# Kernel tuning notes

Measured on AMD Instinct MI355X. Metric: run time of the kernel, lower is better.

## Reference

```python
import jax, jax.numpy as jnp
import numpy as np


def _gcn_layer(h, src, dst, dinv_src_dst, num_nodes, W, b):
    # h: [N, Fin]; src/dst: [E'] (self-loops included); returns [N, Fout]
    h = h @ W  # GCNConv applies the linear transform before propagation
    msg = dinv_src_dst[:, None] * h[src]  # [E', Fout]
    out = jnp.zeros((num_nodes, h.shape[1]), h.dtype).at[dst].add(msg)
    return out + b


def setup_inputs() -> dict:
    key = jax.random.key(0)
    ks = jax.random.split(key, 8)
    N, E, G = 100000, 1600000, 512
    Fin, H, Fout = 1, 64, 16
    x = jax.random.normal(ks[0], (N, Fin), dtype=jnp.float32)
    edge_index = jax.random.randint(ks[1], (2, E), 0, N, dtype=jnp.int64)
    batch = jnp.sort(jax.random.randint(ks[2], (N,), 0, G, dtype=jnp.int64))
    # Glorot-style params (scaled normals are fine for a numerical reference)
    W1 = jax.random.normal(ks[3], (Fin, H), dtype=jnp.float32) / np.sqrt(Fin)
    b1 = jnp.zeros((H,), jnp.float32)
    W2 = jax.random.normal(ks[4], (H, H), dtype=jnp.float32) / np.sqrt(H)
    b2 = jnp.zeros((H,), jnp.float32)
    Wf = jax.random.normal(ks[5], (H, Fout), dtype=jnp.float32) / np.sqrt(H)
    bf = jnp.zeros((Fout,), jnp.float32)
    return {"x": x, "edge_index": edge_index, "batch": batch, "num_graphs": G,
            "W1": W1, "b1": b1, "W2": W2, "b2": b2, "Wf": Wf, "bf": bf}


def reference(x, edge_index, batch, num_graphs, W1, b1, W2, b2, Wf, bf):
    N = x.shape[0]
    loops = jnp.arange(N, dtype=edge_index.dtype)
    src = jnp.concatenate([edge_index[0], loops])  # add self-loops (GCNConv default)
    dst = jnp.concatenate([edge_index[1], loops])
    # symmetric normalization: deg^{-1/2}[src] * deg^{-1/2}[dst]
    deg = jnp.zeros((N,), x.dtype).at[dst].add(1.0)
    dinv = jax.lax.rsqrt(deg)
    norm = dinv[src] * dinv[dst]  # [E']

    h = _gcn_layer(x, src, dst, norm, N, W1, b1)
    h = jax.nn.relu(h)
    h = _gcn_layer(h, src, dst, norm, N, W2, b2)

    # global_mean_pool over batch segments
    sums = jax.ops.segment_sum(h, batch, num_segments=num_graphs)  # [G, H]
    cnts = jax.ops.segment_sum(jnp.ones((N,), h.dtype), batch, num_segments=num_graphs)
    pooled = sums / jnp.maximum(cnts, 1.0)[:, None]
    return pooled @ Wf + bf  # [G, 16]
```

## Files before the change

### kernel.cpp

```cpp
#include <hip/hip_runtime.h>
#include <hip/hip_fp16.h>

#define TPB 256
#define NBUCK 512
#define BCAP 4480
#define A2_BLOCKS 400


__global__ void k_setup(int* cursor, const float* W2, const float* Wf,
                        const float* b2, const float* bf, float* M, float* bb,
                        float* zeroReg, int nzero) {
    int tid = blockIdx.x * blockDim.x + threadIdx.x;
    if (tid < NBUCK) {
        cursor[tid] = tid * BCAP;
    } else if (tid < NBUCK + 1024) {
        int t = tid - NBUCK;
        int f = t >> 4, o = t & 15;
        float a = 0.f;
        for (int k = 0; k < 64; ++k) a = fmaf(W2[f * 64 + k], Wf[k * 16 + o], a);
        M[t] = a;
        if (t < 16) {
            float c = 0.f;
            for (int k = 0; k < 64; ++k) c = fmaf(b2[k], Wf[k * 16 + t], c);
            bb[t] = c + bf[t];
        }
    } else {
        int z = tid - NBUCK - 1024;
        if (z < nzero) zeroReg[z] = 0.f;
    }
}

__global__ void k_bscatter(const int* src, const int* dst, int* bucketCursor,
                           int* packed, int E, int chunk) {
    __shared__ int shc[NBUCK];
    __shared__ int cur[NBUCK];
    int t = threadIdx.x;
    shc[t] = 0; shc[t + 256] = 0;
    __syncthreads();
    int e0 = blockIdx.x * chunk;
    int e1 = min(E, e0 + chunk);
    for (int e = e0 + t; e < e1; e += 256)
        atomicAdd(&shc[dst[e] >> 8], 1);
    __syncthreads();
    int c0 = shc[t], c1 = shc[t + 256];
    if (c0) cur[t] = atomicAdd(&bucketCursor[t], c0);
    if (c1) cur[t + 256] = atomicAdd(&bucketCursor[t + 256], c1);
    __syncthreads();
    for (int e = e0 + t; e < e1; e += 256) {
        int d = dst[e];
        int b = d >> 8;
        int off = atomicAdd(&cur[b], 1);
        if (off < (b + 1) * BCAP)
            packed[off] = ((d & 255) << 24) | src[e];
    }
}

__global__ void k_scan_counts(const int* cursor, int* csrBase) {
    __shared__ int sh[NBUCK];
    int t = threadIdx.x;
    int v = min(cursor[t] - t * BCAP, BCAP);
    sh[t] = v;
    __syncthreads();
    for (int off = 1; off < NBUCK; off <<= 1) {
        int a = (t >= off) ? sh[t - off] : 0;
        __syncthreads();
        sh[t] += a;
        __syncthreads();
    }
    csrBase[t] = sh[t] - v;
    if (t == NBUCK - 1) csrBase[NBUCK] = sh[t];
}

__global__ void k_bucket_csr(const int* cursor, const int* csrBase,
                             const int* packed, const float* x,
                             int* cnt, int* rowStart, float* dinv, float* u,
                             int* csr, int N) {
    __shared__ int c256[256];
    __shared__ int row256[256];
    __shared__ int cur256[256];
    const int b = blockIdx.x;
    const int t = threadIdx.x;
    const int nodeBase = b * 256;
    const int nodeCnt = min(N - nodeBase, 256);
    const int eb = b * BCAP;
    const int ee = min(cursor[b], eb + BCAP);
    const int cb = csrBase[b];

    c256[t] = 0;
    __syncthreads();
    for (int e = eb + t; e < ee; e += 256)
        atomicAdd(&c256[((unsigned)packed[e]) >> 24], 1);
    __syncthreads();

    int v = c256[t];
    row256[t] = v;
    __syncthreads();
    for (int off = 1; off < 256; off <<= 1) {
        int a = (t >= off) ? row256[t - off] : 0;
        __syncthreads();
        row256[t] += a;
        __syncthreads();
    }
    int excl = row256[t] - v;
    cur256[t] = excl;
    __syncthreads();

    if (t < nodeCnt) {
        int i = nodeBase + t;
        cnt[i] = v;
        rowStart[i] = cb + excl;
        float dv = rsqrtf(1.f + (float)v);
        dinv[i] = dv;
        u[i] = dv * x[i];
    }

    for (int e = eb + t; e < ee; e += 256) {
        int w = packed[e];
        int local = ((unsigned)w) >> 24;
        int s = w & 0x00FFFFFF;
        int off = atomicAdd(&cur256[local], 1);
        csr[cb + off] = s;
    }
}

__global__ void k_node(const int* rowStart, const int* cnt, const int* csr,
                       const float* u, const float* dinv,
                       const float* W1, const float* b1, const float* M,
                       __half2* zd, int N) {
    __shared__ float sW1[64], sb1[64], sM[1024];
    int t = threadIdx.x;
    if (t < 64) { sW1[t] = W1[t]; sb1[t] = b1[t]; }
    for (int j = t; j < 1024; j += blockDim.x) sM[j] = M[j];
    __syncthreads();
    int i = blockIdx.x * blockDim.x + t;
    if (i >= N) return;
    float dv = dinv[i];
    int rs = rowStart[i], dg = cnt[i];
    int dgm1 = dg - 1;
    float acc[8];
    acc[0] = u[i];
#pragma unroll
    for (int l = 1; l < 8; ++l) acc[l] = 0.f;
    for (int k = 0; k < dg; k += 16) {
        int sidx[16];
#pragma unroll
        for (int l = 0; l < 16; ++l) sidx[l] = csr[rs + min(k + l, dgm1)];
        float vv[16];
#pragma unroll
        for (int l = 0; l < 16; ++l) vv[l] = u[sidx[l]];
#pragma unroll
        for (int l = 0; l < 16; ++l) acc[l & 7] += (k + l < dg) ? vv[l] : 0.f;
    }
    float s = dv * (((acc[0] + acc[1]) + (acc[2] + acc[3])) +
                    ((acc[4] + acc[5]) + (acc[6] + acc[7])));
    float za[16];
#pragma unroll
    for (int o = 0; o < 16; ++o) za[o] = 0.f;
    for (int f = 0; f < 64; ++f) {
        float hf = fmaxf(fmaf(s, sW1[f], sb1[f]), 0.f);
#pragma unroll
        for (int o = 0; o < 16; ++o) za[o] = fmaf(hf, sM[f * 16 + o], za[o]);
    }
#pragma unroll
    for (int o = 0; o < 8; ++o)
        zd[i * 8 + o] = __floats2half2_rn(dv * za[2 * o], dv * za[2 * o + 1]);
}

__global__ void k_gather_pool(const int* batch, const int* rowStart, const int* cnt,
                              const int* csr, const __half2* zd, const float* dinv,
                              float* gsum, float* cntf, int N) {
    const int t = threadIdx.x;
    const int lane = t & 63, wave = t >> 6;
    const int j = lane & 7, row = lane >> 3;
    const int iw0 = blockIdx.x * 32 + wave * 8;
    const int i = iw0 + row;
    const bool valid = i < N;
    float vx = 0.f, vy = 0.f;
    int g = 0;
    if (valid) {
        g = batch[i];
        int rs = rowStart[i], dg = cnt[i];
        int dgm1 = dg - 1;
        float2 a[8];
        a[0] = __half22float2(zd[i * 8 + j]);
#pragma unroll
        for (int l = 1; l < 8; ++l) a[l] = make_float2(0.f, 0.f);
        for (int k = 0; k < dg; k += 16) {
            int sidx[16];
#pragma unroll
            for (int l = 0; l < 16; ++l) sidx[l] = csr[rs + min(k + l, dgm1)];
            float2 h[16];
#pragma unroll
            for (int l = 0; l < 16; ++l) h[l] = __half22float2(zd[sidx[l] * 8 + j]);
#pragma unroll
            for (int l = 0; l < 16; ++l) {
                bool m = (k + l) < dg;
                a[l & 7].x += m ? h[l].x : 0.f;
                a[l & 7].y += m ? h[l].y : 0.f;
            }
        }
        float dvv = dinv[i];
        vx = dvv * (((a[0].x + a[1].x) + (a[2].x + a[3].x)) +
                    ((a[4].x + a[5].x) + (a[6].x + a[7].x)));
        vy = dvv * (((a[0].y + a[1].y) + (a[2].y + a[3].y)) +
                    ((a[4].y + a[5].y) + (a[6].y + a[7].y)));
    }

    if (iw0 >= N) return;
    const int nvalid = min(N - iw0, 8);
    const int g0 = batch[iw0];
    const int g1 = batch[min(iw0 + 7, N - 1)];

    if (g0 == g1) {
#pragma unroll
        for (int m = 8; m < 64; m <<= 1) {
            vx += __shfl_xor(vx, m);
            vy += __shfl_xor(vy, m);
        }
        if (lane < 8) {
            atomicAdd(&gsum[g0 * 16 + 2 * j],     vx);
            atomicAdd(&gsum[g0 * 16 + 2 * j + 1], vy);
            if (lane == 0) atomicAdd(&cntf[g0], (float)nvalid);
        }
    } else {
        if (valid) {
            atomicAdd(&gsum[g * 16 + 2 * j],     vx);
            atomicAdd(&gsum[g * 16 + 2 * j + 1], vy);
            if (j == 0) atomicAdd(&cntf[g], 1.0f);
        }
    }
}

__global__ void k_final(const float* gsum, const float* cntf, const float* bb,
                        float* out, int G) {
    int t = blockIdx.x * blockDim.x + threadIdx.x;
    int g = t >> 4, o = t & 15;
    if (g >= G) return;
    out[t] = gsum[t] / fmaxf(cntf[g], 1.0f) + bb[o];
}


static inline int cdiv(int a, int b) { return (a + b - 1) / b; }

extern "C" void kernel_launch(void* const* d_in, const int* in_sizes, int n_in,
                              void* d_out, int out_size, void* d_ws, size_t ws_size,
                              hipStream_t stream) {
    const float* x   = (const float*)d_in[0];
    const int*   ei  = (const int*)d_in[1];
    const int*   bat = (const int*)d_in[2];
    const float* W1  = (const float*)d_in[4];
    const float* b1  = (const float*)d_in[5];
    const float* W2  = (const float*)d_in[6];
    const float* b2  = (const float*)d_in[7];
    const float* Wf  = (const float*)d_in[8];
    const float* bf  = (const float*)d_in[9];
    float* out = (float*)d_out;

    const int N = in_sizes[0];
    const int E = in_sizes[1] / 2;
    const int G = out_size / 16;
    const int NB = cdiv(N, 256);

    const int* src = ei;
    const int* dst = ei + E;

    char* w = (char*)d_ws;
    int*   cursor  = (int*)w;           w += NBUCK * 4;
    int*   csrBase = (int*)w;           w += (NBUCK + 1) * 4 + 12;
    int*   packed  = (int*)w;
    __half2* zd    = (__half2*)packed;
    {
        size_t pk = (size_t)NB * BCAP;
        size_t zo = (size_t)8 * N;
        w += (pk > zo ? pk : zo) * 4;
    }
    int*   csr      = (int*)w;          w += (size_t)E * 4;
    int*   cnt      = (int*)w;          w += (size_t)N * 4;
    int*   rowStart = (int*)w;          w += (size_t)N * 4;
    float* dinv     = (float*)w;        w += (size_t)N * 4;
    float* u        = (float*)w;        w += (size_t)N * 4;
    float* gsum     = (float*)w;        w += (size_t)16 * G * 4;
    float* cntf     = (float*)w;        w += (size_t)G * 4;
    float* M        = (float*)w;        w += 1024 * 4;
    float* bb       = (float*)w;

    const int nzero = 16 * G + G;
    const int chunk = cdiv(E, A2_BLOCKS);

    k_setup<<<cdiv(NBUCK + 1024 + nzero, TPB), TPB, 0, stream>>>(
        cursor, W2, Wf, b2, bf, M, bb, gsum, nzero);

    k_bscatter<<<A2_BLOCKS, 256, 0, stream>>>(src, dst, cursor, packed, E, chunk);
    k_scan_counts<<<1, NBUCK, 0, stream>>>(cursor, csrBase);
    k_bucket_csr<<<NB, 256, 0, stream>>>(cursor, csrBase, packed, x,
                                         cnt, rowStart, dinv, u, csr, N);

    k_node<<<cdiv(N, TPB), TPB, 0, stream>>>(rowStart, cnt, csr, u, dinv, W1, b1, M, zd, N);

    k_gather_pool<<<cdiv(N, 32), 256, 0, stream>>>(bat, rowStart, cnt, csr, zd, dinv, gsum, cntf, N);

    k_final<<<cdiv(G * 16, TPB), TPB, 0, stream>>>(gsum, cntf, bb, out, G);
}
```

Before: 109.8 us.

## Replace CSR build with bucket-local push aggregation in shared memory

Drops the prefix-scan and CSR construction kernels and aggregates directly from the destination-bucketed packed edge list. Layer one stages u in four quarter-chunks in LDS and accumulates per destination with shared atomics. Layer two plus pooling scatters half-precision features into a per-bucket LDS accumulator. This removes the CSR writes and the per-node irregular gathers. In exchange it adds heavy shared-memory atomic traffic, rescans the packed list four times, and uses about 100KB of LDS per block, which may limit occupancy.

```diff
diff --git a/kernel.cpp b/kernel.cpp
--- a/kernel.cpp
+++ b/kernel.cpp
@@ -5,6 +5,7 @@
 #define NBUCK 512
 #define BCAP 4480
 #define A2_BLOCKS 400
+#define QMAX 25088
 
 
 __global__ void k_setup(int* cursor, const float* W2, const float* Wf,
@@ -55,104 +56,63 @@
     }
 }
 
-__global__ void k_scan_counts(const int* cursor, int* csrBase) {
-    __shared__ int sh[NBUCK];
-    int t = threadIdx.x;
-    int v = min(cursor[t] - t * BCAP, BCAP);
-    sh[t] = v;
-    __syncthreads();
-    for (int off = 1; off < NBUCK; off <<= 1) {
-        int a = (t >= off) ? sh[t - off] : 0;
-        __syncthreads();
-        sh[t] += a;
-        __syncthreads();
-    }
-    csrBase[t] = sh[t] - v;
-    if (t == NBUCK - 1) csrBase[NBUCK] = sh[t];
-}
-
-__global__ void k_bucket_csr(const int* cursor, const int* csrBase,
-                             const int* packed, const float* x,
-                             int* cnt, int* rowStart, float* dinv, float* u,
-                             int* csr, int N) {
+__global__ void k_bucket1(const int* cursor, const int* packed, const float* x,
+                          float* dinv, float* u, int N) {
     __shared__ int c256[256];
-    __shared__ int row256[256];
-    __shared__ int cur256[256];
-    const int b = blockIdx.x;
-    const int t = threadIdx.x;
-    const int nodeBase = b * 256;
-    const int nodeCnt = min(N - nodeBase, 256);
+    const int b = blockIdx.x, t = threadIdx.x;
     const int eb = b * BCAP;
     const int ee = min(cursor[b], eb + BCAP);
-    const int cb = csrBase[b];
-
     c256[t] = 0;
     __syncthreads();
     for (int e = eb + t; e < ee; e += 256)
         atomicAdd(&c256[((unsigned)packed[e]) >> 24], 1);
     __syncthreads();
-
-    int v = c256[t];
-    row256[t] = v;
-    __syncthreads();
-    for (int off = 1; off < 256; off <<= 1) {
-        int a = (t >= off) ? row256[t - off] : 0;
-        __syncthreads();
-        row256[t] += a;
-        __syncthreads();
-    }
-    int excl = row256[t] - v;
-    cur256[t] = excl;
-    __syncthreads();
-
-    if (t < nodeCnt) {
-        int i = nodeBase + t;
-        cnt[i] = v;
-        rowStart[i] = cb + excl;
-        float dv = rsqrtf(1.f + (float)v);
+    int i = b * 256 + t;
+    if (i < N) {
+        float dv = rsqrtf(1.f + (float)c256[t]);
         dinv[i] = dv;
         u[i] = dv * x[i];
     }
-
-    for (int e = eb + t; e < ee; e += 256) {
-        int w = packed[e];
-        int local = ((unsigned)w) >> 24;
-        int s = w & 0x00FFFFFF;
-        int off = atomicAdd(&cur256[local], 1);
-        csr[cb + off] = s;
-    }
-}
-
-__global__ void k_node(const int* rowStart, const int* cnt, const int* csr,
-                       const float* u, const float* dinv,
-                       const float* W1, const float* b1, const float* M,
-                       __half2* zd, int N) {
+}
+
+__global__ void k_bucket2(const int* cursor, const int* packed,
+                          const float* u, const float* dinv,
+                          const float* W1, const float* b1, const float* M,
+                          __half2* zd, int N, int QN) {
+    __shared__ float uL[QMAX];
+    __shared__ float sacc[256];
     __shared__ float sW1[64], sb1[64], sM[1024];
-    int t = threadIdx.x;
+    const int b = blockIdx.x, t = threadIdx.x;
     if (t < 64) { sW1[t] = W1[t]; sb1[t] = b1[t]; }
-    for (int j = t; j < 1024; j += blockDim.x) sM[j] = M[j];
-    __syncthreads();
-    int i = blockIdx.x * blockDim.x + t;
+    for (int q = t; q < 1024; q += 512) sM[q] = M[q];
+    if (t < 256) sacc[t] = 0.f;
+    const int eb = b * BCAP;
+    const int ee = min(cursor[b], eb + BCAP);
+
+    for (int q = 0; q < 4; ++q) {
+        const int base = q * QN;
+        __syncthreads();
+        for (int idx = t; idx < QN; idx += 512) {
+            int gidx = base + idx;
+            uL[idx] = (gidx < N) ? u[gidx] : 0.f;
+        }
+        __syncthreads();
+        for (int e = eb + t; e < ee; e += 512) {
+            int pk = packed[e];
+            int srcn = pk & 0xFFFFFF;
+            unsigned local = ((unsigned)pk) >> 24;
+            int rel = srcn - base;
+            if ((unsigned)rel < (unsigned)QN)
+                atomicAdd(&sacc[local], uL[rel]);
+        }
+    }
+    __syncthreads();
+
+    if (t >= 256) return;
+    int i = b * 256 + t;
     if (i >= N) return;
     float dv = dinv[i];
-    int rs = rowStart[i], dg = cnt[i];
-    int dgm1 = dg - 1;
-    float acc[8];
-    acc[0] = u[i];
-#pragma unroll
-    for (int l = 1; l < 8; ++l) acc[l] = 0.f;
-    for (int k = 0; k < dg; k += 16) {
-        int sidx[16];
-#pragma unroll
-        for (int l = 0; l < 16; ++l) sidx[l] = csr[rs + min(k + l, dgm1)];
-        float vv[16];
-#pragma unroll
-        for (int l = 0; l < 16; ++l) vv[l] = u[sidx[l]];
-#pragma unroll
-        for (int l = 0; l < 16; ++l) acc[l & 7] += (k + l < dg) ? vv[l] : 0.f;
-    }
-    float s = dv * (((acc[0] + acc[1]) + (acc[2] + acc[3])) +
-                    ((acc[4] + acc[5]) + (acc[6] + acc[7])));
+    float s = dv * (u[i] + sacc[t]);
     float za[16];
 #pragma unroll
     for (int o = 0; o < 16; ++o) za[o] = 0.f;
@@ -163,70 +123,79 @@
     }
 #pragma unroll
     for (int o = 0; o < 8; ++o)
-        zd[i * 8 + o] = __floats2half2_rn(dv * za[2 * o], dv * za[2 * o + 1]);
-}
-
-__global__ void k_gather_pool(const int* batch, const int* rowStart, const int* cnt,
-                              const int* csr, const __half2* zd, const float* dinv,
-                              float* gsum, float* cntf, int N) {
-    const int t = threadIdx.x;
+        zd[(size_t)i * 8 + o] = __floats2half2_rn(dv * za[2 * o], dv * za[2 * o + 1]);
+}
+
+__global__ void k_bucketpool(const int* cursor, const int* packed, const int* batch,
+                             const float* dinv, const __half2* zd,
+                             float* gsum, float* cntf, int N) {
+    __shared__ float acc[256][17];
+    const int b = blockIdx.x, t = threadIdx.x;
+    float* accf = &acc[0][0];
+    for (int q = t; q < 256 * 17; q += 512) accf[q] = 0.f;
+    __syncthreads();
+
+    const int eb = b * BCAP;
+    const int ee = min(cursor[b], eb + BCAP);
+    const int j = t & 7, grp = t >> 3;
+
+    int e = eb + grp;
+    for (; e + 64 < ee; e += 128) {
+        int pk0 = packed[e], pk1 = packed[e + 64];
+        int s0 = pk0 & 0xFFFFFF, s1 = pk1 & 0xFFFFFF;
+        unsigned l0 = ((unsigned)pk0) >> 24, l1 = ((unsigned)pk1) >> 24;
+        float2 f0 = __half22float2(zd[(size_t)s0 * 8 + j]);
+        float2 f1 = __half22float2(zd[(size_t)s1 * 8 + j]);
+        atomicAdd(&acc[l0][2 * j],     f0.x);
+        atomicAdd(&acc[l0][2 * j + 1], f0.y);
+        atomicAdd(&acc[l1][2 * j],     f1.x);
+        atomicAdd(&acc[l1][2 * j + 1], f1.y);
+    }
+    for (; e < ee; e += 64) {
+        int pk = packed[e];
+        int s0 = pk & 0xFFFFFF;
+        unsigned l0 = ((unsigned)pk) >> 24;
+        float2 f0 = __half22float2(zd[(size_t)s0 * 8 + j]);
+        atomicAdd(&acc[l0][2 * j],     f0.x);
+        atomicAdd(&acc[l0][2 * j + 1], f0.y);
+    }
+    __syncthreads();
+
     const int lane = t & 63, wave = t >> 6;
-    const int j = lane & 7, row = lane >> 3;
-    const int iw0 = blockIdx.x * 32 + wave * 8;
-    const int i = iw0 + row;
-    const bool valid = i < N;
-    float vx = 0.f, vy = 0.f;
-    int g = 0;
-    if (valid) {
-        g = batch[i];
-        int rs = rowStart[i], dg = cnt[i];
-        int dgm1 = dg - 1;
-        float2 a[8];
-        a[0] = __half22float2(zd[i * 8 + j]);
-#pragma unroll
-        for (int l = 1; l < 8; ++l) a[l] = make_float2(0.f, 0.f);
-        for (int k = 0; k < dg; k += 16) {
-            int sidx[16];
-#pragma unroll
-            for (int l = 0; l < 16; ++l) sidx[l] = csr[rs + min(k + l, dgm1)];
-            float2 h[16];
-#pragma unroll
-            for (int l = 0; l < 16; ++l) h[l] = __half22float2(zd[sidx[l] * 8 + j]);
-#pragma unroll
-            for (int l = 0; l < 16; ++l) {
-                bool m = (k + l) < dg;
-                a[l & 7].x += m ? h[l].x : 0.f;
-                a[l & 7].y += m ? h[l].y : 0.f;
+    const int jr = lane & 7, row = lane >> 3;
+    for (int r = 0; r < 4; ++r) {
+        int n0 = wave * 8 + r * 64;
+        int i0 = b * 256 + n0;
+        if (i0 >= N) continue;
+        int i = i0 + row;
+        bool valid = i < N;
+        float vx = 0.f, vy = 0.f;
+        int g = 0;
+        if (valid) {
+            g = batch[i];
+            float2 zo = __half22float2(zd[(size_t)i * 8 + jr]);
+            float dvv = dinv[i];
+            vx = dvv * (acc[n0 + row][2 * jr]     + zo.x);
+            vy = dvv * (acc[n0 + row][2 * jr + 1] + zo.y);
+        }
+        int nvalid = min(N - i0, 8);
+        int g0 = batch[i0];
+        int g1 = batch[min(i0 + 7, N - 1)];
+        if (g0 == g1) {
+#pragma unroll
+            for (int m = 8; m < 64; m <<= 1) {
+                vx += __shfl_xor(vx, m);
+                vy += __shfl_xor(vy, m);
             }
-        }
-        float dvv = dinv[i];
-        vx = dvv * (((a[0].x + a[1].x) + (a[2].x + a[3].x)) +
-                    ((a[4].x + a[5].x) + (a[6].x + a[7].x)));
-        vy = dvv * (((a[0].y + a[1].y) + (a[2].y + a[3].y)) +
-                    ((a[4].y + a[5].y) + (a[6].y + a[7].y)));
-    }
-
-    if (iw0 >= N) return;
-    const int nvalid = min(N - iw0, 8);
-    const int g0 = batch[iw0];
-    const int g1 = batch[min(iw0 + 7, N - 1)];
-
-    if (g0 == g1) {
-#pragma unroll
-        for (int m = 8; m < 64; m <<= 1) {
-            vx += __shfl_xor(vx, m);
-            vy += __shfl_xor(vy, m);
-        }
-        if (lane < 8) {
-            atomicAdd(&gsum[g0 * 16 + 2 * j],     vx);
-            atomicAdd(&gsum[g0 * 16 + 2 * j + 1], vy);
-            if (lane == 0) atomicAdd(&cntf[g0], (float)nvalid);
-        }
-    } else {
-        if (valid) {
-            atomicAdd(&gsum[g * 16 + 2 * j],     vx);
-            atomicAdd(&gsum[g * 16 + 2 * j + 1], vy);
-            if (j == 0) atomicAdd(&cntf[g], 1.0f);
+            if (lane < 8) {
+                atomicAdd(&gsum[g0 * 16 + 2 * jr],     vx);
+                atomicAdd(&gsum[g0 * 16 + 2 * jr + 1], vy);
+                if (lane == 0) atomicAdd(&cntf[g0], (float)nvalid);
+            }
+        } else if (valid) {
+            atomicAdd(&gsum[g * 16 + 2 * jr],     vx);
+            atomicAdd(&gsum[g * 16 + 2 * jr + 1], vy);
+            if (jr == 0) atomicAdd(&cntf[g], 1.0f);
         }
     }
 }
@@ -260,29 +229,22 @@
     const int E = in_sizes[1] / 2;
     const int G = out_size / 16;
     const int NB = cdiv(N, 256);
+    int QN = ((cdiv(N, 4) + 511) / 512) * 512;
+    if (QN > QMAX) QN = QMAX;
 
     const int* src = ei;
     const int* dst = ei + E;
 
     char* w = (char*)d_ws;
-    int*   cursor  = (int*)w;           w += NBUCK * 4;
-    int*   csrBase = (int*)w;           w += (NBUCK + 1) * 4 + 12;
-    int*   packed  = (int*)w;
-    __half2* zd    = (__half2*)packed;
-    {
-        size_t pk = (size_t)NB * BCAP;
-        size_t zo = (size_t)8 * N;
-        w += (pk > zo ? pk : zo) * 4;
-    }
-    int*   csr      = (int*)w;          w += (size_t)E * 4;
-    int*   cnt      = (int*)w;          w += (size_t)N * 4;
-    int*   rowStart = (int*)w;          w += (size_t)N * 4;
-    float* dinv     = (float*)w;        w += (size_t)N * 4;
-    float* u        = (float*)w;        w += (size_t)N * 4;
-    float* gsum     = (float*)w;        w += (size_t)16 * G * 4;
-    float* cntf     = (float*)w;        w += (size_t)G * 4;
-    float* M        = (float*)w;        w += 1024 * 4;
-    float* bb       = (float*)w;
+    int*     cursor = (int*)w;          w += NBUCK * 4;
+    int*     packed = (int*)w;          w += (size_t)NBUCK * BCAP * 4;
+    __half2* zd     = (__half2*)w;      w += (size_t)8 * N * 4;
+    float*   dinv   = (float*)w;        w += (size_t)N * 4;
+    float*   u      = (float*)w;        w += (size_t)N * 4;
+    float*   gsum   = (float*)w;        w += (size_t)16 * G * 4;
+    float*   cntf   = (float*)w;        w += (size_t)G * 4;
+    float*   M      = (float*)w;        w += 1024 * 4;
+    float*   bb     = (float*)w;
 
     const int nzero = 16 * G + G;
     const int chunk = cdiv(E, A2_BLOCKS);
@@ -291,13 +253,12 @@
         cursor, W2, Wf, b2, bf, M, bb, gsum, nzero);
 
     k_bscatter<<<A2_BLOCKS, 256, 0, stream>>>(src, dst, cursor, packed, E, chunk);
-    k_scan_counts<<<1, NBUCK, 0, stream>>>(cursor, csrBase);
-    k_bucket_csr<<<NB, 256, 0, stream>>>(cursor, csrBase, packed, x,
-                                         cnt, rowStart, dinv, u, csr, N);
-
-    k_node<<<cdiv(N, TPB), TPB, 0, stream>>>(rowStart, cnt, csr, u, dinv, W1, b1, M, zd, N);
-
-    k_gather_pool<<<cdiv(N, 32), 256, 0, stream>>>(bat, rowStart, cnt, csr, zd, dinv, gsum, cntf, N);
+
+    k_bucket1<<<NB, 256, 0, stream>>>(cursor, packed, x, dinv, u, N);
+
+    k_bucket2<<<NB, 512, 0, stream>>>(cursor, packed, u, dinv, W1, b1, M, zd, N, QN);
+
+    k_bucketpool<<<NB, 512, 0, stream>>>(cursor, packed, bat, dinv, zd, gsum, cntf, N);
 
     k_final<<<cdiv(G * 16, TPB), TPB, 0, stream>>>(gsum, cntf, bb, out, G);
 }
```

Result: slower. 324.4 us (+195.5%).
